# Performance work log

Hardware: AMD Instinct MI355X
Metric: run time of the kernel (lower is better)

The kernel has to match this reference:

```python
import jax, jax.numpy as jnp
import numpy as np
import math

NUM_HEADS = 8
DIM = 512
DH = DIM // NUM_HEADS  # 64


def _rotary(x):
    # x: (b, l, h, s, d) ; interleaved-pair rotary (lucidrains RotaryEmbedding default)
    d = x.shape[-1]
    s = x.shape[-2]
    inv_freq = 1.0 / (10000.0 ** (jnp.arange(0, d, 2, dtype=jnp.float32) / d))  # (d/2,)
    t = jnp.arange(s, dtype=jnp.float32)
    freqs = t[:, None] * inv_freq[None, :]                # (s, d/2)
    freqs = jnp.repeat(freqs, 2, axis=-1)                 # (s, d) interleaved duplication
    cos = jnp.cos(freqs).astype(x.dtype)
    sin = jnp.sin(freqs).astype(x.dtype)
    x1 = x[..., 0::2]
    x2 = x[..., 1::2]
    rot = jnp.stack([-x2, x1], axis=-1).reshape(x.shape)  # rotate_half on interleaved pairs
    return x * cos + rot * sin


def setup_inputs() -> dict:
    key = jax.random.key(0)
    ks = jax.random.split(key, 9)
    b, l, s = 2, 2, 2048
    std = 1.0 / math.sqrt(DIM)
    inp = {
        "x": jax.random.normal(ks[0], (b, l, s, DIM), dtype=jnp.float32),
        "Wq": jax.random.normal(ks[1], (DIM, DIM), dtype=jnp.float32) * std,
        "bq": jnp.zeros((DIM,), dtype=jnp.float32),
        "Wk": jax.random.normal(ks[2], (DIM, DIM), dtype=jnp.float32) * std,
        "bk": jnp.zeros((DIM,), dtype=jnp.float32),
        "Wv": jax.random.normal(ks[3], (DIM, DIM), dtype=jnp.float32) * std,
        "bv": jnp.zeros((DIM,), dtype=jnp.float32),
        "Wo": jax.random.normal(ks[4], (DIM, DIM), dtype=jnp.float32) * std,
        "bo": jnp.zeros((DIM,), dtype=jnp.float32),
    }
    return inp


def reference(x, Wq, bq, Wk, bk, Wv, bv, Wo, bo):
    b, l, s, _ = x.shape
    h, dh = NUM_HEADS, DH

    def proj(W, bias):
        y = jnp.einsum('blsd,ed->blse', x, W) + bias      # nn.Linear: x @ W.T + b
        return y.reshape(b, l, s, h, dh).transpose(0, 1, 3, 2, 4)  # b l h s d

    q_proj = proj(Wq, bq)
    k_proj = proj(Wk, bk)
    v_proj = proj(Wv, bv)

    # Faithful to the source's swapped tuple unpack: k_mat <- V projection, v_mat <- K projection
    q_mat = _rotary(q_proj)
    k_mat = _rotary(v_proj)
    v_mat = k_proj

    scale = 1.0 / math.sqrt(dh * h)  # sqrt(dim), as in source
    scores = jnp.einsum('blhqd,blhkd->blhqk', q_mat, k_mat) * scale

    causal = jnp.tril(jnp.ones((s, s), dtype=bool))
    scores = jnp.where(causal[None, None, None], scores, -jnp.inf)

    weights = jax.nn.softmax(scores, axis=-1)
    inter = jnp.einsum('blhqk,blhkd->blhqd', weights, v_mat)
    inter = inter.transpose(0, 1, 3, 2, 4).reshape(b, l, s, h * dh)  # b l s (h d)
    out = jnp.einsum('blse,de->blsd', inter, Wo) + bo
    return out
```

## Files before the change

### kernel.cpp

```cpp
#include <hip/hip_runtime.h>
#include <math.h>

#define BB 2
#define LL 2
#define SS 2048
#define DD 512
#define HH 8
#define DHH 64

typedef __attribute__((ext_vector_type(8))) short bf16x8;
typedef __attribute__((ext_vector_type(4))) float f32x4;

#define MFMA16(a, b, c) __builtin_amdgcn_mfma_f32_16x16x32_bf16((a), (b), (c), 0, 0, 0)

#if __has_builtin(__builtin_amdgcn_exp2f)
#define EXP2F(x) __builtin_amdgcn_exp2f(x)
#else
#define EXP2F(x) exp2f(x)
#endif

__device__ __forceinline__ unsigned short f2bf(float f) {
    union { float f; unsigned u; } x; x.f = f;
    unsigned u = x.u;
    return (unsigned short)((u + 0x7fffu + ((u >> 16) & 1u)) >> 16);
}

__device__ __forceinline__ void gload16(const unsigned short* g, unsigned short* l) {
    __builtin_amdgcn_global_load_lds(
        (const __attribute__((address_space(1))) unsigned int*)g,
        (__attribute__((address_space(3))) unsigned int*)l, 16, 0, 0);
}

__global__ __launch_bounds__(256) void prep_kernel(
    const float* __restrict__ x,  const float* __restrict__ wq,
    const float* __restrict__ wk, const float* __restrict__ wv,
    const float* __restrict__ wo, unsigned short* __restrict__ dst,
    float* __restrict__ cos_t, float* __restrict__ sin_t)
{
    int i = blockIdx.x * 256 + threadIdx.x;
    if (i < 1310720) {
        const float* src;
        int local;
        if (i < 1048576)      { src = x;  local = i; }
        else if (i < 1114112) { src = wq; local = i - 1048576; }
        else if (i < 1179648) { src = wk; local = i - 1114112; }
        else if (i < 1245184) { src = wv; local = i - 1179648; }
        else                  { src = wo; local = i - 1245184; }
        float4 v = ((const float4*)src)[local];
        ushort4 o;
        o.x = f2bf(v.x); o.y = f2bf(v.y); o.z = f2bf(v.z); o.w = f2bf(v.w);
        *(ushort4*)&dst[(size_t)i * 4] = o;
    } else {
        int idx = i - 1310720;
        int s = idx >> 5;
        int f = idx & 31;
        double inv = pow(10000.0, -(double)(2 * f) / (double)DHH);
        double ang = (double)s * inv;
        cos_t[idx] = (float)cos(ang);
        sin_t[idx] = (float)sin(ang);
    }
}

__global__ __launch_bounds__(256) void qkv_mfma_kernel(
    const unsigned short* __restrict__ xb,
    const unsigned short* __restrict__ wqb,
    const unsigned short* __restrict__ wkb,
    const unsigned short* __restrict__ wvb,
    const float* __restrict__ bq, const float* __restrict__ bk,
    const float* __restrict__ bv,
    const float* __restrict__ cos_t, const float* __restrict__ sin_t,
    unsigned short* __restrict__ qm, unsigned short* __restrict__ km,
    unsigned short* __restrict__ vt)
{
    __shared__ __align__(16) unsigned short As[2][4096];
    __shared__ __align__(16) unsigned short Bs[2][4096];

    const int tid  = threadIdx.x;
    const int w    = tid >> 6;
    const int lane = tid & 63;
    const int c    = lane & 15;
    const int quad = lane >> 4;
    const int mw   = (w & 1) * 64;
    const int nw   = (w >> 1) * 64;

    const int bx    = blockIdx.x;
    const int mat   = bx >> 2;
    const int nloc0 = (bx & 3) * 128;
    const int row0  = blockIdx.y * 128;

    const unsigned short* wsel = (mat == 0) ? wqb : (mat == 1) ? wkb : wvb;
    const float* bsel          = (mat == 0) ? bq  : (mat == 1) ? bk  : bv;

    const unsigned short* aSrc = (mat == 1) ? (wsel + (size_t)nloc0 * DD)
                                            : (xb   + (size_t)row0  * DD);
    const unsigned short* bSrc = (mat == 1) ? (xb   + (size_t)row0  * DD)
                                            : (wsel + (size_t)nloc0 * DD);

    auto stage = [&](int k0, int bb) {
        #pragma unroll
        for (int it = 0; it < 2; ++it) {
            int L   = it * 256 + tid;
            int row = L >> 2;
            int k8  = (L & 3) * 8;
            gload16(aSrc + (size_t)row * DD + k0 + k8, &As[bb][L * 8]);
            gload16(bSrc + (size_t)row * DD + k0 + k8, &Bs[bb][L * 8]);
        }
    };

    f32x4 acc[4][4];
    #pragma unroll
    for (int i = 0; i < 4; ++i)
        #pragma unroll
        for (int j = 0; j < 4; ++j)
            #pragma unroll
            for (int r = 0; r < 4; ++r) acc[i][j][r] = 0.f;

    stage(0, 0);
    __syncthreads();

    for (int k0 = 0; k0 < DD; k0 += 32) {
        const int bb = (k0 >> 5) & 1;
        if (k0 + 32 < DD) stage(k0 + 32, bb ^ 1);

        bf16x8 af[4], bfr[4];
        #pragma unroll
        for (int mt = 0; mt < 4; ++mt)
            af[mt] = *(const bf16x8*)&As[bb][(mw + mt * 16 + c) * 32 + quad * 8];
        #pragma unroll
        for (int nt = 0; nt < 4; ++nt)
            bfr[nt] = *(const bf16x8*)&Bs[bb][(nw + nt * 16 + c) * 32 + quad * 8];
        #pragma unroll
        for (int mt = 0; mt < 4; ++mt)
            #pragma unroll
            for (int nt = 0; nt < 4; ++nt)
                acc[mt][nt] = MFMA16(af[mt], bfr[nt], acc[mt][nt]);

        __syncthreads();
    }

    if (mat == 1) {
        #pragma unroll
        for (int mt = 0; mt < 4; ++mt) {
            #pragma unroll
            for (int nt = 0; nt < 4; ++nt) {
                int xr = row0 + nw + nt * 16 + c;
                int bl = xr >> 11, s = xr & 2047;
                #pragma unroll
                for (int r = 0; r < 4; ++r) {
                    int col = nloc0 + mw + mt * 16 + quad * 4 + r;
                    int h = col >> 6, dh = col & 63;
                    float v = acc[mt][nt][r] + bsel[col];
                    vt[((size_t)(bl * HH + h) * DHH + dh) * SS + s] = f2bf(v);
                }
            }
        }
    } else {
        unsigned short* dst = (mat == 0) ? qm : km;
        const float qscale = (mat == 0) ? 0.06375871448932861f : 1.0f;
        #pragma unroll
        for (int mt = 0; mt < 4; ++mt) {
            #pragma unroll
            for (int r = 0; r < 4; ++r) {
                int xr = row0 + mw + mt * 16 + quad * 4 + r;
                int bl = xr >> 11, s = xr & 2047;
                #pragma unroll
                for (int nt = 0; nt < 4; ++nt) {
                    int col = nloc0 + nw + nt * 16 + c;
                    int h = col >> 6, dh = col & 63;
                    float v = acc[mt][nt][r] + bsel[col];
                    float pv = __shfl_xor(v, 1);
                    int f = dh >> 1;
                    float cs = cos_t[s * 32 + f], sn = sin_t[s * 32 + f];
                    float o = (dh & 1) ? fmaf(v, cs, pv * sn)
                                       : fmaf(v, cs, -(pv * sn));
                    dst[((size_t)(bl * HH + h) * SS + s) * DHH + dh] = f2bf(o * qscale);
                }
            }
        }
    }
}

#define S_P 72

__global__ __launch_bounds__(128) void attn_mfma_kernel(
    const unsigned short* __restrict__ qm,
    const unsigned short* __restrict__ km,
    const unsigned short* __restrict__ vt,
    unsigned short* __restrict__ inter)
{
    __shared__ __align__(16) unsigned short Ks[2][4096];
    __shared__ __align__(16) unsigned short Vs[2][4096];
    __shared__ __align__(16) unsigned short Ps[64 * S_P];

    const int tid  = threadIdx.x;
    const int w    = tid >> 6;
    const int lane = tid & 63;
    const int c    = lane & 15;
    const int quad = lane >> 4;

    const int h  = blockIdx.x;
    const int qt = 31 - blockIdx.y;
    const int bl = blockIdx.z;
    const int qw = qt * 64 + w * 32;

    const size_t seq_base = (size_t)(bl * HH + h) * SS * DHH;
    const size_t vt_base  = (size_t)(bl * HH + h) * DHH * SS;

    bf16x8 qf[2][2];
    #pragma unroll
    for (int nt = 0; nt < 2; ++nt)
        #pragma unroll
        for (int kk = 0; kk < 2; ++kk)
            qf[nt][kk] = *(const bf16x8*)(qm + seq_base +
                (size_t)(qw + nt * 16 + c) * DHH + kk * 32 + quad * 8);

    f32x4 oacc[4][2];
    f32x4 lacc[2];
    #pragma unroll
    for (int i = 0; i < 4; ++i)
        #pragma unroll
        for (int j = 0; j < 2; ++j)
            #pragma unroll
            for (int r = 0; r < 4; ++r) oacc[i][j][r] = 0.f;
    #pragma unroll
    for (int j = 0; j < 2; ++j)
        #pragma unroll
        for (int r = 0; r < 4; ++r) lacc[j][r] = 0.f;

    bf16x8 ones;
    #pragma unroll
    for (int i = 0; i < 8; ++i) ones[i] = (short)0x3F80;

    auto stage = [&](int kt, int bb) {
        const unsigned short* kg = km + seq_base + (size_t)(kt << 6) * DHH;
        const unsigned short* vg = vt + vt_base + (kt << 6);
        #pragma unroll
        for (int it = 0; it < 4; ++it) {
            int L   = it * 128 + tid;
            int row = L >> 3;
            int gch = (L & 7) ^ (row & 7);
            gload16(kg + row * DHH + gch * 8, &Ks[bb][L * 8]);
            gload16(vg + (size_t)row * SS + gch * 8, &Vs[bb][L * 8]);
        }
    };

    const int ntiles = qt + 1;
    stage(0, 0);
    __syncthreads();

    for (int kt = 0; kt < ntiles; ++kt) {
        const int bb = kt & 1;
        if (kt + 1 < ntiles) stage(kt + 1, bb ^ 1);

        f32x4 sacc[4][2];
        #pragma unroll
        for (int mt = 0; mt < 4; ++mt)
            #pragma unroll
            for (int nt = 0; nt < 2; ++nt)
                #pragma unroll
                for (int r = 0; r < 4; ++r) sacc[mt][nt][r] = 0.f;
        #pragma unroll
        for (int kk = 0; kk < 2; ++kk) {
            bf16x8 kf[4];
            #pragma unroll
            for (int mt = 0; mt < 4; ++mt) {
                int rr = mt * 16 + c;
                kf[mt] = *(const bf16x8*)&Ks[bb][rr * 64 +
                    (((kk * 4 + quad) ^ (rr & 7)) * 8)];
            }
            #pragma unroll
            for (int mt = 0; mt < 4; ++mt)
                #pragma unroll
                for (int nt = 0; nt < 2; ++nt)
                    sacc[mt][nt] = MFMA16(kf[mt], qf[nt][kk], sacc[mt][nt]);
        }

        const bool need_mask = (64 * kt + 63 > qw);
        #pragma unroll
        for (int mt = 0; mt < 4; ++mt) {
            #pragma unroll
            for (int nt = 0; nt < 2; ++nt) {
                int q = qw + nt * 16 + c;
                unsigned u[4];
                #pragma unroll
                for (int r = 0; r < 4; ++r) {
                    float p = EXP2F(sacc[mt][nt][r]);
                    if (need_mask) {
                        int key = kt * 64 + mt * 16 + quad * 4 + r;
                        if (key > q) p = 0.f;
                    }
                    union { float f; unsigned u; } cv; cv.f = p;
                    u[r] = cv.u + 0x8000u;
                }
                uint2 d;
                d.x = __builtin_amdgcn_perm(u[1], u[0], 0x07060302u);
                d.y = __builtin_amdgcn_perm(u[3], u[2], 0x07060302u);
                *(uint2*)&Ps[(w * 32 + nt * 16 + c) * S_P + mt * 16 + quad * 4] = d;
            }
        }

        #pragma unroll
        for (int kk = 0; kk < 2; ++kk) {
            bf16x8 bp[2];
            #pragma unroll
            for (int nt = 0; nt < 2; ++nt) {
                bp[nt] = *(const bf16x8*)&Ps[(w * 32 + nt * 16 + c) * S_P +
                                             kk * 32 + quad * 8];
                lacc[nt] = MFMA16(ones, bp[nt], lacc[nt]);
            }
            #pragma unroll
            for (int mt4 = 0; mt4 < 4; ++mt4) {
                int rv = mt4 * 16 + c;
                bf16x8 av = *(const bf16x8*)&Vs[bb][rv * 64 +
                    (((kk * 4 + quad) ^ (rv & 7)) * 8)];
                oacc[mt4][0] = MFMA16(av, bp[0], oacc[mt4][0]);
                oacc[mt4][1] = MFMA16(av, bp[1], oacc[mt4][1]);
            }
        }

        __syncthreads();
    }

    float invl0 = 1.f / lacc[0][0];
    float invl1 = 1.f / lacc[1][0];
    #pragma unroll
    for (int mt4 = 0; mt4 < 4; ++mt4) {
        int dh0 = mt4 * 16 + quad * 4;
        #pragma unroll
        for (int nt = 0; nt < 2; ++nt) {
            int query = qw + nt * 16 + c;
            float il = nt ? invl1 : invl0;
            ushort4 o;
            o.x = f2bf(oacc[mt4][nt][0] * il);
            o.y = f2bf(oacc[mt4][nt][1] * il);
            o.z = f2bf(oacc[mt4][nt][2] * il);
            o.w = f2bf(oacc[mt4][nt][3] * il);
            *(ushort4*)&inter[((size_t)bl * SS + query) * DD + h * DHH + dh0] = o;
        }
    }
}

__global__ __launch_bounds__(256) void outproj_mfma_kernel(
    const unsigned short* __restrict__ ib,
    const unsigned short* __restrict__ wob,
    const float* __restrict__ bo, float* __restrict__ out)
{
    __shared__ __align__(16) unsigned short As[2][4096];
    __shared__ __align__(16) unsigned short Bs[2][2048];

    const int tid  = threadIdx.x;
    const int w    = tid >> 6;
    const int lane = tid & 63;
    const int c    = lane & 15;
    const int quad = lane >> 4;
    const int mw   = (w & 1) * 64;
    const int nw   = (w >> 1) * 32;

    const int n0   = blockIdx.x * 64;
    const int row0 = blockIdx.y * 128;

    const unsigned short* aSrc = ib  + (size_t)row0 * DD;
    const unsigned short* bSrc = wob + (size_t)n0   * DD;

    auto stage = [&](int k0, int bb) {
        #pragma unroll
        for (int it = 0; it < 2; ++it) {
            int L = it * 256 + tid;
            gload16(aSrc + (size_t)(L >> 2) * DD + k0 + (L & 3) * 8,
                    &As[bb][L * 8]);
        }
        int L = tid;
        gload16(bSrc + (size_t)(L >> 2) * DD + k0 + (L & 3) * 8,
                &Bs[bb][L * 8]);
    };

    f32x4 acc[4][2];
    #pragma unroll
    for (int i = 0; i < 4; ++i)
        #pragma unroll
        for (int j = 0; j < 2; ++j)
            #pragma unroll
            for (int r = 0; r < 4; ++r) acc[i][j][r] = 0.f;

    stage(0, 0);
    __syncthreads();

    for (int k0 = 0; k0 < DD; k0 += 32) {
        const int bb = (k0 >> 5) & 1;
        if (k0 + 32 < DD) stage(k0 + 32, bb ^ 1);

        bf16x8 af[4], bfr[2];
        #pragma unroll
        for (int mt = 0; mt < 4; ++mt)
            af[mt] = *(const bf16x8*)&As[bb][(mw + mt * 16 + c) * 32 + quad * 8];
        #pragma unroll
        for (int nt = 0; nt < 2; ++nt)
            bfr[nt] = *(const bf16x8*)&Bs[bb][(nw + nt * 16 + c) * 32 + quad * 8];
        #pragma unroll
        for (int mt = 0; mt < 4; ++mt)
            #pragma unroll
            for (int nt = 0; nt < 2; ++nt)
                acc[mt][nt] = MFMA16(af[mt], bfr[nt], acc[mt][nt]);

        __syncthreads();
    }

    #pragma unroll
    for (int mt = 0; mt < 4; ++mt) {
        #pragma unroll
        for (int r = 0; r < 4; ++r) {
            int xr = row0 + mw + mt * 16 + quad * 4 + r;
            #pragma unroll
            for (int nt = 0; nt < 2; ++nt) {
                int col = n0 + nw + nt * 16 + c;
                out[(size_t)xr * DD + col] = acc[mt][nt][r] + bo[col];
            }
        }
    }
}

extern "C" void kernel_launch(void* const* d_in, const int* in_sizes, int n_in,
                              void* d_out, int out_size, void* d_ws, size_t ws_size,
                              hipStream_t stream)
{
    const float* x  = (const float*)d_in[0];
    const float* Wq = (const float*)d_in[1];
    const float* bq = (const float*)d_in[2];
    const float* Wk = (const float*)d_in[3];
    const float* bk = (const float*)d_in[4];
    const float* Wv = (const float*)d_in[5];
    const float* bv = (const float*)d_in[6];
    const float* Wo = (const float*)d_in[7];
    const float* bo = (const float*)d_in[8];
    float* out = (float*)d_out;
    char* ws = (char*)d_ws;

    unsigned short* inter = (unsigned short*)(ws);
    float* cos_t = (float*)(ws + 8388608);
    float* sin_t = (float*)(ws + 8650752);
    unsigned short* xb  = (unsigned short*)(ws + 8912896);
    unsigned short* wqb = (unsigned short*)(ws + 17301504);
    unsigned short* wkb = (unsigned short*)(ws + 17825792);
    unsigned short* wvb = (unsigned short*)(ws + 18350080);
    unsigned short* wob = (unsigned short*)(ws + 18874368);
    unsigned short* qm  = (unsigned short*)(ws + 19398656);
    unsigned short* km  = (unsigned short*)(ws + 27787264);
    unsigned short* vt  = (unsigned short*)(ws + 36175872);

    prep_kernel<<<dim3(5376), dim3(256), 0, stream>>>(
        x, Wq, Wk, Wv, Wo, xb, cos_t, sin_t);
    qkv_mfma_kernel<<<dim3(12, 64), dim3(256), 0, stream>>>(
        xb, wqb, wkb, wvb, bq, bk, bv, cos_t, sin_t, qm, km, vt);
    attn_mfma_kernel<<<dim3(HH, 32, BB * LL), dim3(128), 0, stream>>>(qm, km, vt, inter);
    outproj_mfma_kernel<<<dim3(8, 64), dim3(256), 0, stream>>>(inter, wob, bo, out);
}
```

Baseline: 195.7 us.

## Vectorize projection epilogues and enlarge attention query tile to 128 rows

The QKV and output-projection GEMMs swap operand roles so each lane holds four consecutive output columns or sequence positions. This lets the epilogues write packed ushort4/float4 stores, and the rotary step is applied in-register without cross-lane shuffles. The attention kernel moves to 256 threads per block with 128-row query tiles, so each staged K/V tile is shared by four waves and the grid is halved. Waves whose rows are fully masked for a key tile skip its compute but still join the staging and barriers. Bf16 rounding in the new pack path uses round-half-up rather than round-to-nearest-even, which changes the numerics slightly.

```diff
diff --git a/kernel.cpp b/kernel.cpp
--- a/kernel.cpp
+++ b/kernel.cpp
@@ -23,6 +23,20 @@
     union { float f; unsigned u; } x; x.f = f;
     unsigned u = x.u;
     return (unsigned short)((u + 0x7fffu + ((u >> 16) & 1u)) >> 16);
+}
+
+__device__ __forceinline__ unsigned bcast(float f) {
+    union { float f; unsigned u; } x; x.f = f;
+    return x.u;
+}
+
+__device__ __forceinline__ ushort4 pack4(float a, float b, float c, float d) {
+    unsigned u0 = bcast(a) + 0x8000u, u1 = bcast(b) + 0x8000u;
+    unsigned u2 = bcast(c) + 0x8000u, u3 = bcast(d) + 0x8000u;
+    union { uint2 v; ushort4 s; } r;
+    r.v.x = __builtin_amdgcn_perm(u1, u0, 0x07060302u);
+    r.v.y = __builtin_amdgcn_perm(u3, u2, 0x07060302u);
+    return r.s;
 }
 
 __device__ __forceinline__ void gload16(const unsigned short* g, unsigned short* l) {
@@ -91,10 +105,10 @@
     const unsigned short* wsel = (mat == 0) ? wqb : (mat == 1) ? wkb : wvb;
     const float* bsel          = (mat == 0) ? bq  : (mat == 1) ? bk  : bv;
 
-    const unsigned short* aSrc = (mat == 1) ? (wsel + (size_t)nloc0 * DD)
+    const unsigned short* aSrc = (mat == 1) ? (xb   + (size_t)row0  * DD)
+                                            : (wsel + (size_t)nloc0 * DD);
+    const unsigned short* bSrc = (mat == 1) ? (wsel + (size_t)nloc0 * DD)
                                             : (xb   + (size_t)row0  * DD);
-    const unsigned short* bSrc = (mat == 1) ? (xb   + (size_t)row0  * DD)
-                                            : (wsel + (size_t)nloc0 * DD);
 
     auto stage = [&](int k0, int bb) {
         #pragma unroll
@@ -140,49 +154,51 @@
 
     if (mat == 1) {
         #pragma unroll
+        for (int nt = 0; nt < 4; ++nt) {
+            int col = nloc0 + nw + nt * 16 + c;
+            int h = col >> 6, dh = col & 63;
+            float bias = bsel[col];
+            #pragma unroll
+            for (int mt = 0; mt < 4; ++mt) {
+                int xr0 = row0 + mw + mt * 16 + quad * 4;
+                int bl = xr0 >> 11, s0 = xr0 & 2047;
+                ushort4 o = pack4(acc[mt][nt][0] + bias, acc[mt][nt][1] + bias,
+                                  acc[mt][nt][2] + bias, acc[mt][nt][3] + bias);
+                *(ushort4*)&vt[((size_t)(bl * HH + h) * DHH + dh) * SS + s0] = o;
+            }
+        }
+    } else {
+        unsigned short* dst = (mat == 0) ? qm : km;
+        const float qscale = (mat == 0) ? 0.06375871448932861f : 1.0f;
+        #pragma unroll
         for (int mt = 0; mt < 4; ++mt) {
+            int col0 = nloc0 + mw + mt * 16 + quad * 4;
+            int h = col0 >> 6, dh0 = col0 & 63;
+            int f0 = dh0 >> 1;
+            float4 bias4 = *(const float4*)&bsel[col0];
             #pragma unroll
             for (int nt = 0; nt < 4; ++nt) {
                 int xr = row0 + nw + nt * 16 + c;
                 int bl = xr >> 11, s = xr & 2047;
-                #pragma unroll
-                for (int r = 0; r < 4; ++r) {
-                    int col = nloc0 + mw + mt * 16 + quad * 4 + r;
-                    int h = col >> 6, dh = col & 63;
-                    float v = acc[mt][nt][r] + bsel[col];
-                    vt[((size_t)(bl * HH + h) * DHH + dh) * SS + s] = f2bf(v);
-                }
+                float2 cs = *(const float2*)&cos_t[s * 32 + f0];
+                float2 sn = *(const float2*)&sin_t[s * 32 + f0];
+                float c0 = cs.x * qscale, s0v = sn.x * qscale;
+                float c1 = cs.y * qscale, s1v = sn.y * qscale;
+                float v0 = acc[mt][nt][0] + bias4.x;
+                float v1 = acc[mt][nt][1] + bias4.y;
+                float v2 = acc[mt][nt][2] + bias4.z;
+                float v3 = acc[mt][nt][3] + bias4.w;
+                ushort4 o = pack4(v0 * c0 - v1 * s0v, v1 * c0 + v0 * s0v,
+                                  v2 * c1 - v3 * s1v, v3 * c1 + v2 * s1v);
+                *(ushort4*)&dst[((size_t)(bl * HH + h) * SS + s) * DHH + dh0] = o;
             }
         }
-    } else {
-        unsigned short* dst = (mat == 0) ? qm : km;
-        const float qscale = (mat == 0) ? 0.06375871448932861f : 1.0f;
-        #pragma unroll
-        for (int mt = 0; mt < 4; ++mt) {
-            #pragma unroll
-            for (int r = 0; r < 4; ++r) {
-                int xr = row0 + mw + mt * 16 + quad * 4 + r;
-                int bl = xr >> 11, s = xr & 2047;
-                #pragma unroll
-                for (int nt = 0; nt < 4; ++nt) {
-                    int col = nloc0 + nw + nt * 16 + c;
-                    int h = col >> 6, dh = col & 63;
-                    float v = acc[mt][nt][r] + bsel[col];
-                    float pv = __shfl_xor(v, 1);
-                    int f = dh >> 1;
-                    float cs = cos_t[s * 32 + f], sn = sin_t[s * 32 + f];
-                    float o = (dh & 1) ? fmaf(v, cs, pv * sn)
-                                       : fmaf(v, cs, -(pv * sn));
-                    dst[((size_t)(bl * HH + h) * SS + s) * DHH + dh] = f2bf(o * qscale);
-                }
-            }
-        }
     }
 }
 
 #define S_P 72
 
-__global__ __launch_bounds__(128) void attn_mfma_kernel(
+__global__ __launch_bounds__(256, 2) void attn_mfma_kernel(
     const unsigned short* __restrict__ qm,
     const unsigned short* __restrict__ km,
     const unsigned short* __restrict__ vt,
@@ -190,7 +206,7 @@
 {
     __shared__ __align__(16) unsigned short Ks[2][4096];
     __shared__ __align__(16) unsigned short Vs[2][4096];
-    __shared__ __align__(16) unsigned short Ps[64 * S_P];
+    __shared__ __align__(16) unsigned short Ps[128 * S_P];
 
     const int tid  = threadIdx.x;
     const int w    = tid >> 6;
@@ -199,9 +215,9 @@
     const int quad = lane >> 4;
 
     const int h  = blockIdx.x;
-    const int qt = 31 - blockIdx.y;
+    const int qt = 15 - blockIdx.y;
     const int bl = blockIdx.z;
-    const int qw = qt * 64 + w * 32;
+    const int qw = qt * 128 + w * 32;
 
     const size_t seq_base = (size_t)(bl * HH + h) * SS * DHH;
     const size_t vt_base  = (size_t)(bl * HH + h) * DHH * SS;
@@ -231,93 +247,95 @@
     #pragma unroll
     for (int i = 0; i < 8; ++i) ones[i] = (short)0x3F80;
 
-    auto stage = [&](int kt, int bb) {
-        const unsigned short* kg = km + seq_base + (size_t)(kt << 6) * DHH;
-        const unsigned short* vg = vt + vt_base + (kt << 6);
-        #pragma unroll
-        for (int it = 0; it < 4; ++it) {
-            int L   = it * 128 + tid;
+    const int ntiles = 2 * qt + 2;
+
+    auto stage = [&](int kt, int b) {
+        const unsigned short* kg = km + seq_base + (size_t)(kt * 64) * DHH;
+        const unsigned short* vg = vt + vt_base + kt * 64;
+        #pragma unroll
+        for (int it = 0; it < 2; ++it) {
+            int L   = it * 256 + tid;
             int row = L >> 3;
             int gch = (L & 7) ^ (row & 7);
-            gload16(kg + row * DHH + gch * 8, &Ks[bb][L * 8]);
-            gload16(vg + (size_t)row * SS + gch * 8, &Vs[bb][L * 8]);
+            gload16(kg + row * DHH + gch * 8, &Ks[b][L * 8]);
+            gload16(vg + (size_t)row * SS + gch * 8, &Vs[b][L * 8]);
         }
     };
 
-    const int ntiles = qt + 1;
     stage(0, 0);
     __syncthreads();
 
     for (int kt = 0; kt < ntiles; ++kt) {
-        const int bb = kt & 1;
-        if (kt + 1 < ntiles) stage(kt + 1, bb ^ 1);
-
-        f32x4 sacc[4][2];
-        #pragma unroll
-        for (int mt = 0; mt < 4; ++mt)
-            #pragma unroll
-            for (int nt = 0; nt < 2; ++nt)
-                #pragma unroll
-                for (int r = 0; r < 4; ++r) sacc[mt][nt][r] = 0.f;
-        #pragma unroll
-        for (int kk = 0; kk < 2; ++kk) {
-            bf16x8 kf[4];
+        const int b = kt & 1;
+        const int ktn = (kt + 1 < ntiles) ? kt + 1 : kt;
+        stage(ktn, b ^ 1);
+
+        if (64 * kt <= qw + 31) {
+            f32x4 sacc[4][2];
+            #pragma unroll
+            for (int mt = 0; mt < 4; ++mt)
+                #pragma unroll
+                for (int nt = 0; nt < 2; ++nt)
+                    #pragma unroll
+                    for (int r = 0; r < 4; ++r) sacc[mt][nt][r] = 0.f;
+            #pragma unroll
+            for (int kk = 0; kk < 2; ++kk) {
+                bf16x8 kf[4];
+                #pragma unroll
+                for (int mt = 0; mt < 4; ++mt) {
+                    int rr = mt * 16 + c;
+                    kf[mt] = *(const bf16x8*)&Ks[b][rr * 64 +
+                        (((kk * 4 + quad) ^ (rr & 7)) * 8)];
+                }
+                #pragma unroll
+                for (int mt = 0; mt < 4; ++mt)
+                    #pragma unroll
+                    for (int nt = 0; nt < 2; ++nt)
+                        sacc[mt][nt] = MFMA16(kf[mt], qf[nt][kk], sacc[mt][nt]);
+            }
+
+            const bool need_mask = (64 * kt + 63 > qw);
             #pragma unroll
             for (int mt = 0; mt < 4; ++mt) {
-                int rr = mt * 16 + c;
-                kf[mt] = *(const bf16x8*)&Ks[bb][rr * 64 +
-                    (((kk * 4 + quad) ^ (rr & 7)) * 8)];
+                #pragma unroll
+                for (int nt = 0; nt < 2; ++nt) {
+                    int q = qw + nt * 16 + c;
+                    unsigned u[4];
+                    #pragma unroll
+                    for (int r = 0; r < 4; ++r) {
+                        float p = EXP2F(sacc[mt][nt][r]);
+                        if (need_mask) {
+                            int key = kt * 64 + mt * 16 + quad * 4 + r;
+                            if (key > q) p = 0.f;
+                        }
+                        u[r] = bcast(p) + 0x8000u;
+                    }
+                    uint2 d;
+                    d.x = __builtin_amdgcn_perm(u[1], u[0], 0x07060302u);
+                    d.y = __builtin_amdgcn_perm(u[3], u[2], 0x07060302u);
+                    *(uint2*)&Ps[(w * 32 + nt * 16 + c) * S_P + mt * 16 + quad * 4] = d;
+                }
             }
-            #pragma unroll
-            for (int mt = 0; mt < 4; ++mt)
-                #pragma unroll
-                for (int nt = 0; nt < 2; ++nt)
-                    sacc[mt][nt] = MFMA16(kf[mt], qf[nt][kk], sacc[mt][nt]);
-        }
-
-        const bool need_mask = (64 * kt + 63 > qw);
-        #pragma unroll
-        for (int mt = 0; mt < 4; ++mt) {
-            #pragma unroll
-            for (int nt = 0; nt < 2; ++nt) {
-                int q = qw + nt * 16 + c;
-                unsigned u[4];
-                #pragma unroll
-                for (int r = 0; r < 4; ++r) {
-                    float p = EXP2F(sacc[mt][nt][r]);
-                    if (need_mask) {
-                        int key = kt * 64 + mt * 16 + quad * 4 + r;
-                        if (key > q) p = 0.f;
-                    }
-                    union { float f; unsigned u; } cv; cv.f = p;
-                    u[r] = cv.u + 0x8000u;
+
+            #pragma unroll
+            for (int kk = 0; kk < 2; ++kk) {
+                bf16x8 bp[2];
+                #pragma unroll
+                for (int nt = 0; nt < 2; ++nt) {
+                    bp[nt] = *(const bf16x8*)&Ps[(w * 32 + nt * 16 + c) * S_P +
+                                                 kk * 32 + quad * 8];
+                    lacc[nt] = MFMA16(ones, bp[nt], lacc[nt]);
                 }
-                uint2 d;
-                d.x = __builtin_amdgcn_perm(u[1], u[0], 0x07060302u);
-                d.y = __builtin_amdgcn_perm(u[3], u[2], 0x07060302u);
-                *(uint2*)&Ps[(w * 32 + nt * 16 + c) * S_P + mt * 16 + quad * 4] = d;
+                #pragma unroll
+                for (int mt4 = 0; mt4 < 4; ++mt4) {
+                    int rv = mt4 * 16 + c;
+                    bf16x8 av = *(const bf16x8*)&Vs[b][rv * 64 +
+                        (((kk * 4 + quad) ^ (rv & 7)) * 8)];
+                    oacc[mt4][0] = MFMA16(av, bp[0], oacc[mt4][0]);
+                    oacc[mt4][1] = MFMA16(av, bp[1], oacc[mt4][1]);
+                }
             }
         }
-
-        #pragma unroll
-        for (int kk = 0; kk < 2; ++kk) {
-            bf16x8 bp[2];
-            #pragma unroll
-            for (int nt = 0; nt < 2; ++nt) {
-                bp[nt] = *(const bf16x8*)&Ps[(w * 32 + nt * 16 + c) * S_P +
-                                             kk * 32 + quad * 8];
-                lacc[nt] = MFMA16(ones, bp[nt], lacc[nt]);
-            }
-            #pragma unroll
-            for (int mt4 = 0; mt4 < 4; ++mt4) {
-                int rv = mt4 * 16 + c;
-                bf16x8 av = *(const bf16x8*)&Vs[bb][rv * 64 +
-                    (((kk * 4 + quad) ^ (rv & 7)) * 8)];
-                oacc[mt4][0] = MFMA16(av, bp[0], oacc[mt4][0]);
-                oacc[mt4][1] = MFMA16(av, bp[1], oacc[mt4][1]);
-            }
-        }
-
         __syncthreads();
     }
 
@@ -345,40 +363,40 @@
     const unsigned short* __restrict__ wob,
     const float* __restrict__ bo, float* __restrict__ out)
 {
-    __shared__ __align__(16) unsigned short As[2][4096];
-    __shared__ __align__(16) unsigned short Bs[2][2048];
+    __shared__ __align__(16) unsigned short As[2][2048];
+    __shared__ __align__(16) unsigned short Bs[2][4096];
 
     const int tid  = threadIdx.x;
     const int w    = tid >> 6;
     const int lane = tid & 63;
     const int c    = lane & 15;
     const int quad = lane >> 4;
-    const int mw   = (w & 1) * 64;
-    const int nw   = (w >> 1) * 32;
+    const int mw   = (w & 1) * 32;
+    const int nw   = (w >> 1) * 64;
 
     const int n0   = blockIdx.x * 64;
     const int row0 = blockIdx.y * 128;
 
-    const unsigned short* aSrc = ib  + (size_t)row0 * DD;
-    const unsigned short* bSrc = wob + (size_t)n0   * DD;
+    const unsigned short* aSrc = wob + (size_t)n0   * DD;
+    const unsigned short* bSrc = ib  + (size_t)row0 * DD;
 
     auto stage = [&](int k0, int bb) {
+        int L = tid;
+        gload16(aSrc + (size_t)(L >> 2) * DD + k0 + (L & 3) * 8,
+                &As[bb][L * 8]);
         #pragma unroll
         for (int it = 0; it < 2; ++it) {
-            int L = it * 256 + tid;
-            gload16(aSrc + (size_t)(L >> 2) * DD + k0 + (L & 3) * 8,
-                    &As[bb][L * 8]);
-        }
-        int L = tid;
-        gload16(bSrc + (size_t)(L >> 2) * DD + k0 + (L & 3) * 8,
-                &Bs[bb][L * 8]);
+            int L2 = it * 256 + tid;
+            gload16(bSrc + (size_t)(L2 >> 2) * DD + k0 + (L2 & 3) * 8,
+                    &Bs[bb][L2 * 8]);
+        }
     };
 
-    f32x4 acc[4][2];
-    #pragma unroll
-    for (int i = 0; i < 4; ++i)
-        #pragma unroll
-        for (int j = 0; j < 2; ++j)
+    f32x4 acc[2][4];
+    #pragma unroll
+    for (int i = 0; i < 2; ++i)
+        #pragma unroll
+        for (int j = 0; j < 4; ++j)
             #pragma unroll
             for (int r = 0; r < 4; ++r) acc[i][j][r] = 0.f;
 
@@ -389,32 +407,35 @@
         const int bb = (k0 >> 5) & 1;
         if (k0 + 32 < DD) stage(k0 + 32, bb ^ 1);
 
-        bf16x8 af[4], bfr[2];
-        #pragma unroll
-        for (int mt = 0; mt < 4; ++mt)
+        bf16x8 af[2], bfr[4];
+        #pragma unroll
+        for (int mt = 0; mt < 2; ++mt)
             af[mt] = *(const bf16x8*)&As[bb][(mw + mt * 16 + c) * 32 + quad * 8];
         #pragma unroll
-        for (int nt = 0; nt < 2; ++nt)
+        for (int nt = 0; nt < 4; ++nt)
             bfr[nt] = *(const bf16x8*)&Bs[bb][(nw + nt * 16 + c) * 32 + quad * 8];
         #pragma unroll
-        for (int mt = 0; mt < 4; ++mt)
-            #pragma unroll
-            for (int nt = 0; nt < 2; ++nt)
+        for (int mt = 0; mt < 2; ++mt)
+            #pragma unroll
+            for (int nt = 0; nt < 4; ++nt)
                 acc[mt][nt] = MFMA16(af[mt], bfr[nt], acc[mt][nt]);
 
         __syncthreads();
     }
 
     #pragma unroll
-    for (int mt = 0; mt < 4; ++mt) {
-        #pragma unroll
-        for (int r = 0; r < 4; ++r) {
-            int xr = row0 + mw + mt * 16 + quad * 4 + r;
-            #pragma unroll
-            for (int nt = 0; nt < 2; ++nt) {
-                int col = n0 + nw + nt * 16 + c;
-                out[(size_t)xr * DD + col] = acc[mt][nt][r] + bo[col];
-            }
+    for (int mt = 0; mt < 2; ++mt) {
+        int col0 = n0 + mw + mt * 16 + quad * 4;
+        float4 b4 = *(const float4*)&bo[col0];
+        #pragma unroll
+        for (int nt = 0; nt < 4; ++nt) {
+            int xr = row0 + nw + nt * 16 + c;
+            float4 o;
+            o.x = acc[mt][nt][0] + b4.x;
+            o.y = acc[mt][nt][1] + b4.y;
+            o.z = acc[mt][nt][2] + b4.z;
+            o.w = acc[mt][nt][3] + b4.w;
+            *(float4*)&out[(size_t)xr * DD + col0] = o;
         }
     }
 }
@@ -451,6 +472,6 @@
         x, Wq, Wk, Wv, Wo, xb, cos_t, sin_t);
     qkv_mfma_kernel<<<dim3(12, 64), dim3(256), 0, stream>>>(
         xb, wqb, wkb, wvb, bq, bk, bv, cos_t, sin_t, qm, km, vt);
-    attn_mfma_kernel<<<dim3(HH, 32, BB * LL), dim3(128), 0, stream>>>(qm, km, vt, inter);
+    attn_mfma_kernel<<<dim3(HH, 16, BB * LL), dim3(256), 0, stream>>>(qm, km, vt, inter);
     outproj_mfma_kernel<<<dim3(8, 64), dim3(256), 0, stream>>>(inter, wob, bo, out);
 }
```

Measured after the change: 199.7 us. 1.02x slower.
